# Kernel optimization log

Hardware: AMD Instinct MI355X
Metric: run time of the kernel (lower is better)

The kernel has to match this reference:

```python
import jax, jax.numpy as jnp
import numpy as np

NN_SIZE = 10  # matches init_kwargs nn_size


def _knn_idx(points, k):
    """points: (B,N,D). Returns (B,N,k) indices of k nearest neighbors, self excluded."""
    sq = jnp.sum(points * points, axis=-1)  # (B,N)
    # squared euclidean distances (B,N,N)
    d2 = sq[:, :, None] + sq[:, None, :] - 2.0 * jnp.einsum('bnd,bmd->bnm', points, points)
    _, idx = jax.lax.top_k(-d2, k + 1)  # smallest distances; first hit is self
    return idx[:, :, 1:]  # drop self -> (B,N,k)


def _uniform_laplacian(points, knn_idx):
    """points: (B,N,D); knn_idx: (B,N,K). lap = mean(neighbors) - point."""
    neigh = jax.vmap(lambda p, i: p[i])(points, knn_idx)  # (B,N,K,D) gather per batch
    return jnp.mean(neigh, axis=2) - points


def setup_inputs() -> dict:
    key = jax.random.key(0)
    k1, k2 = jax.random.split(key)
    B, N, D = 2, 8192, 3
    point1 = jax.random.normal(k1, (B, N, D), dtype=jnp.float32)
    point2 = jax.random.normal(k2, (B, N, D), dtype=jnp.float32)
    return {"point1": point1, "point2": point2}


def reference(point1, point2):
    knn_idx = _knn_idx(point1, NN_SIZE)          # connectivity from ref cloud
    lap1 = _uniform_laplacian(point1, knn_idx)   # (B,N,3)
    lap2 = _uniform_laplacian(point2, knn_idx)   # reuse knn_idx
    # metric = L1Loss (mean reduction); use_norm=False
    return jnp.mean(jnp.abs(lap1 - lap2))
```

## Files before the change

kernel.cpp:

```cpp
#include <hip/hip_runtime.h>
#include <math.h>


constexpr int NPTS  = 8192;
constexpr int NB    = 2;
constexpr int KNN   = 10;
constexpr int QPB   = 64;
constexpr int WPB   = 16;
constexpr int BLOCK = QPB * WPB;
constexpr int MASK13 = 0xFFFFE000;

constexpr int   G    = 32;
constexpr int   NC   = G * G * G;
constexpr float BMIN = -5.5f;
constexpr float BW   = 11.0f;
constexpr float H    = BW / G;
constexpr float INVH = (float)G / BW;

__device__ __forceinline__ void ins1(int l[KNN], int x) {
#pragma unroll
    for (int k = KNN - 1; k > 0; --k) l[k] = min(l[k], max(l[k - 1], x));
    l[0] = min(l[0], x);
}
__device__ __forceinline__ void ins2(int l[KNN], int a, int b) {
    const int b0 = min(a, b), b1 = max(a, b);
#pragma unroll
    for (int k = KNN - 1; k >= 2; --k)
        l[k] = min(l[k], min(max(l[k - 1], b0), max(l[k - 2], b1)));
    l[1] = min(l[1], min(max(l[0], b0), b1));
    l[0] = min(l[0], b0);
}
template<int S>
__device__ __forceinline__ void ins2s(int l[KNN], int a, int b) {
    const int b0 = min(a, b), b1 = max(a, b);
#pragma unroll
    for (int k = KNN - 1; k >= S + 2; --k)
        l[k] = min(l[k], min(max(l[k - 1], b0), max(l[k - 2], b1)));
    l[S + 1] = min(l[S + 1], min(max(l[S], b0), b1));
    l[S] = min(l[S], b0);
}
__device__ __forceinline__ void merge_sorted(int l[KNN], const int p[KNN]) {
    ins2s<0>(l, p[0], p[1]);
    ins2s<2>(l, p[2], p[3]);
    ins2s<4>(l, p[4], p[5]);
    ins2s<6>(l, p[6], p[7]);
    ins2s<8>(l, p[8], p[9]);
}

__global__ void pack_bin(const float* __restrict__ p1, float4* __restrict__ w,
                         int* __restrict__ hist, int* __restrict__ cellof,
                         float* __restrict__ out, int* __restrict__ nfail) {
    const int i = blockIdx.x * blockDim.x + threadIdx.x;
    if (i >= NB * NPTS) return;
    if (i == 0) { out[0] = 0.0f; nfail[0] = 0; }
    const float x = p1[3 * i], y = p1[3 * i + 1], z = p1[3 * i + 2];
    w[i] = make_float4(x, y, z, fmaf(x, x, fmaf(y, y, z * z)));
    const int cx = min(max((int)floorf((x - BMIN) * INVH), 0), G - 1);
    const int cy = min(max((int)floorf((y - BMIN) * INVH), 0), G - 1);
    const int cz = min(max((int)floorf((z - BMIN) * INVH), 0), G - 1);
    const int c = (cz << 10) | (cy << 5) | cx;
    cellof[i] = c;
    atomicAdd(&hist[(i >> 13) * NC + c], 1);
}

__global__ __launch_bounds__(1024)
void scan_cells(const int* __restrict__ hist, int* __restrict__ starts) {
    __shared__ int wsum[16];
    const int b = blockIdx.x, t = threadIdx.x;
    const int* hb = hist + b * NC;
    int* sb = starts + b * (NC + 1);
    const int c0 = t * 32;
    int loc[32]; int sum = 0;
#pragma unroll
    for (int j = 0; j < 32; ++j) { loc[j] = hb[c0 + j]; sum += loc[j]; }
    const int lane = t & 63, wvi = t >> 6;
    int incl = sum;
#pragma unroll
    for (int off = 1; off < 64; off <<= 1) {
        const int v = __shfl_up(incl, off);
        if (lane >= off) incl += v;
    }
    if (lane == 63) wsum[wvi] = incl;
    __syncthreads();
    if (t < 16) {
        const int v = wsum[t];
        int iv = v;
#pragma unroll
        for (int off = 1; off < 16; off <<= 1) {
            const int u = __shfl_up(iv, off);
            if (t >= off) iv += u;
        }
        wsum[t] = iv - v;
    }
    __syncthreads();
    int run = wsum[wvi] + incl - sum;
#pragma unroll
    for (int j = 0; j < 32; ++j) { sb[c0 + j] = run; run += loc[j]; }
    if (t == 1023) sb[NC] = run;
}

__global__ void scatter_all(const int* __restrict__ cellof,
                            const int* __restrict__ starts,
                            int* __restrict__ hist,
                            const float4* __restrict__ w,
                            float4* __restrict__ wsorted,
                            int* __restrict__ sIdx) {
    const int i = blockIdx.x * blockDim.x + threadIdx.x;
    if (i >= NB * NPTS) return;
    const int b = i >> 13;
    const int c = cellof[i];
    const int old = atomicSub(&hist[b * NC + c], 1);
    const int pos = b * NPTS + starts[b * (NC + 1) + c] + old - 1;
    wsorted[pos] = w[i];
    sIdx[pos] = i & (NPTS - 1);
}

template<int S>
__device__ __forceinline__ void scan_batched(const float4* __restrict__ W,
                                             const int* __restrict__ st,
                                             int cx, int cy, int cz,
                                             float m2x, float m2y, float m2z,
                                             float q2, int qpos, int wv,
                                             int l[KNN])
{
    constexpr int Wd = 2 * S + 1;
    constexpr int R  = Wd * Wd;
    const int IMAX = 0x7FFFFFFF;
    int J0[R], J1[R];
#pragma unroll
    for (int r = 0; r < R; ++r) {
        const int dy = r % Wd - S, dz = r / Wd - S;
        const int ay = cy + dy, az = cz + dz;
        const bool ok = ((unsigned)ay < G) && ((unsigned)az < G);
        const int cbase = (az << 10) | (ay << 5);
        const int lo = cbase + max(cx - S, 0);
        const int hi = cbase + min(cx + S, G - 1) + 1;
        J0[r] = ok ? st[lo] : 0;
        J1[r] = ok ? st[hi] : 0;
    }
#pragma unroll
    for (int r = 0; r < R; ++r) {
        const int j1 = J1[r];
        int j = J0[r] + wv;
        if (j < j1) {
            float4 c4 = W[j];
            while (true) {
                const int jn = j + WPB;
                const bool more = jn < j1;
                float4 nx;
                if (more) nx = W[jn];
                const float d2 = fmaf(m2x, c4.x,
                                 fmaf(m2y, c4.y,
                                 fmaf(m2z, c4.z, c4.w + q2)));
                int key = (__float_as_int(d2) & MASK13) | j;
                key = (j == qpos) ? IMAX : key;
                ins1(l, key);
                if (!more) break;
                c4 = nx; j = jn;
            }
        }
    }
}

__global__ __launch_bounds__(BLOCK)
void phase1(const float4* __restrict__ wsorted, const int* __restrict__ sIdx,
            const float* __restrict__ p2, const int* __restrict__ starts,
            float* __restrict__ out,
            int* __restrict__ nfail, int* __restrict__ worklist)
{
    __shared__ int mv[WPB * KNN * QPB];

    const int batch = blockIdx.x >> 7;
    const int lane  = threadIdx.x & 63;
    const int wv    = __builtin_amdgcn_readfirstlane(threadIdx.x >> 6);
    const int qpos  = ((blockIdx.x & 127) << 6) + lane;

    const float4* W  = wsorted + batch * NPTS;
    const int*    sI = sIdx + batch * NPTS;
    const float*  P2 = p2 + (size_t)batch * NPTS * 3;
    const int*    st = starts + batch * (NC + 1);

    const float4 qp = W[qpos];
    const int cx = min(max((int)floorf((qp.x - BMIN) * INVH), 0), G - 1);
    const int cy = min(max((int)floorf((qp.y - BMIN) * INVH), 0), G - 1);
    const int cz = min(max((int)floorf((qp.z - BMIN) * INVH), 0), G - 1);
    const float lox = BMIN + cx * H, loy = BMIN + cy * H, loz = BMIN + cz * H;
    const float df = fminf(fminf(fminf(qp.x - lox, lox + H - qp.x),
                                 fminf(qp.y - loy, loy + H - qp.y)),
                           fminf(qp.z - loz, loz + H - qp.z));
    const float m2x = -2.0f * qp.x, m2y = -2.0f * qp.y, m2z = -2.0f * qp.z;
    const float q2 = qp.w;
    const int IMAX = 0x7FFFFFFF;

    const int sCov = (q2 > 4.8f) ? 2 : 1;

    int l[KNN];
#pragma unroll
    for (int k = 0; k < KNN; ++k) l[k] = IMAX;

    if (sCov == 1)
        scan_batched<1>(W, st, cx, cy, cz, m2x, m2y, m2z, q2, qpos, wv, l);
    else
        scan_batched<2>(W, st, cx, cy, cz, m2x, m2y, m2z, q2, qpos, wv, l);

#pragma unroll
    for (int k = 0; k < KNN; ++k) mv[(wv * KNN + k) * QPB + lane] = l[k];
    __syncthreads();

    if (threadIdx.x < QPB) {
        int M[KNN];
#pragma unroll
        for (int k = 0; k < KNN; ++k) M[k] = IMAX;
#pragma unroll
        for (int e = 0; e < WPB; ++e) {
            int p[KNN];
#pragma unroll
            for (int k = 0; k < KNN; ++k) p[k] = mv[(e * KNN + k) * QPB + lane];
            merge_sorted(M, p);
        }

        const float tau = __int_as_float(M[KNN - 1] & MASK13);
        const float R = (float)sCov * H + df;
        const bool covered = (tau <= R * R * 0.996f);
        float v = 0.0f;
        if (covered) {
            float s1x = 0, s1y = 0, s1z = 0, s2x = 0, s2y = 0, s2z = 0;
#pragma unroll
            for (int k = 0; k < KNN; ++k) {
                const int j = M[k] & (NPTS - 1);
                const float4 c4 = W[j];
                const int oi = sI[j];
                s1x += c4.x; s1y += c4.y; s1z += c4.z;
                s2x += P2[3 * oi + 0];
                s2y += P2[3 * oi + 1];
                s2z += P2[3 * oi + 2];
            }
            const int oq = sI[qpos];
            const float p2x = P2[3 * oq + 0];
            const float p2y = P2[3 * oq + 1];
            const float p2z = P2[3 * oq + 2];
            const float dx = (s1x * 0.1f - qp.x) - (s2x * 0.1f - p2x);
            const float dy = (s1y * 0.1f - qp.y) - (s2y * 0.1f - p2y);
            const float dz = (s1z * 0.1f - qp.z) - (s2z * 0.1f - p2z);
            v = fabsf(dx) + fabsf(dy) + fabsf(dz);
        } else {
            const int wi = atomicAdd(nfail, 1);
            worklist[wi] = (batch << 16) | qpos;
        }
#pragma unroll
        for (int off = 32; off >= 1; off >>= 1) v += __shfl_down(v, off);
        if (threadIdx.x == 0)
            atomicAdd(out, v * (1.0f / (float)(NB * NPTS * 3)));
    }
}

constexpr int P2BLK = 256;
constexpr int P2GRID = 512;

__global__ __launch_bounds__(P2BLK)
void phase2(const float4* __restrict__ wsorted, const int* __restrict__ sIdx,
            const float* __restrict__ p2,
            const int* __restrict__ nfail, const int* __restrict__ worklist,
            float* __restrict__ out)
{
    const int lane = threadIdx.x & 63;
    const int wv   = threadIdx.x >> 6;
    const int wid  = blockIdx.x * (P2BLK / 64) + wv;
    const int NW   = P2GRID * (P2BLK / 64);
    const int nf   = *nfail;
    const int IMAX = 0x7FFFFFFF;
    float acc = 0.0f;

    for (int i = wid; i < nf; i += NW) {
        const int e = worklist[i];
        const int batch = e >> 16, qpos = e & 0xFFFF;
        const float4* W  = wsorted + batch * NPTS;
        const int*    sI = sIdx + batch * NPTS;
        const float*  P2 = p2 + (size_t)batch * NPTS * 3;
        const float4 qp = W[qpos];
        const float m2x = -2.0f * qp.x, m2y = -2.0f * qp.y, m2z = -2.0f * qp.z;
        const float q2 = qp.w;

        int l[KNN];
#pragma unroll
        for (int k = 0; k < KNN; ++k) l[k] = IMAX;

#pragma unroll 2
        for (int it = 0; it < NPTS / 128; ++it) {
            const int ja = it * 128 + lane, jb = ja + 64;
            const float4 ca = W[ja];
            const float4 cb = W[jb];
            const float da = fmaf(m2x, ca.x, fmaf(m2y, ca.y, fmaf(m2z, ca.z, ca.w + q2)));
            const float db = fmaf(m2x, cb.x, fmaf(m2y, cb.y, fmaf(m2z, cb.z, cb.w + q2)));
            int ka = (__float_as_int(da) & MASK13) | ja;
            int kb = (__float_as_int(db) & MASK13) | jb;
            ka = (ja == qpos) ? IMAX : ka;
            kb = (jb == qpos) ? IMAX : kb;
            ins2(l, ka, kb);
        }
        for (int off = 1; off < 64; off <<= 1) {
            int p[KNN];
#pragma unroll
            for (int k = 0; k < KNN; ++k) p[k] = __shfl_xor(l[k], off);
            merge_sorted(l, p);
        }
        float s1x = 0, s1y = 0, s1z = 0, s2x = 0, s2y = 0, s2z = 0;
#pragma unroll
        for (int k = 0; k < KNN; ++k) {
            const int j = l[k] & (NPTS - 1);
            const float4 c4 = W[j];
            const int oi = sI[j];
            s1x += c4.x; s1y += c4.y; s1z += c4.z;
            s2x += P2[3 * oi + 0];
            s2y += P2[3 * oi + 1];
            s2z += P2[3 * oi + 2];
        }
        const int oq = sI[qpos];
        const float dx = (s1x * 0.1f - qp.x) - (s2x * 0.1f - P2[3 * oq + 0]);
        const float dy = (s1y * 0.1f - qp.y) - (s2y * 0.1f - P2[3 * oq + 1]);
        const float dz = (s1z * 0.1f - qp.z) - (s2z * 0.1f - P2[3 * oq + 2]);
        if (lane == 0) acc += fabsf(dx) + fabsf(dy) + fabsf(dz);
    }

    if (lane == 0 && acc != 0.0f)
        atomicAdd(out, acc * (1.0f / (float)(NB * NPTS * 3)));
}

constexpr int FB_WPB = 8;
constexpr int FB_BLOCK = QPB * FB_WPB;
constexpr int CHUNK = NPTS / FB_WPB;

__global__ void prep_pack(const float* __restrict__ p, float4* __restrict__ w) {
    const int i = blockIdx.x * blockDim.x + threadIdx.x;
    if (i < NB * NPTS) {
        const float x = p[3 * i], y = p[3 * i + 1], z = p[3 * i + 2];
        w[i] = make_float4(x, y, z, fmaf(x, x, fmaf(y, y, z * z)));
    }
}

__global__ __launch_bounds__(FB_BLOCK, 2)
void knn_lap(const float4* __restrict__ w1, const float* __restrict__ p2,
             float* __restrict__ out)
{
    __shared__ int mv[FB_WPB * KNN * QPB];
    const int batch = blockIdx.x >> 7;
    const int qbase = (blockIdx.x & 127) << 6;
    const int lane  = threadIdx.x & 63;
    const int wv    = __builtin_amdgcn_readfirstlane(threadIdx.x >> 6);
    const int query = qbase + lane;
    const float4* Wb = w1 + batch * NPTS;
    const float4 qp = Wb[query];
    const float m2x = -2.0f * qp.x, m2y = -2.0f * qp.y, m2z = -2.0f * qp.z;
    const float q2 = qp.w;
    const int IMAX = 0x7FFFFFFF;
    int l[KNN];
#pragma unroll
    for (int k = 0; k < KNN; ++k) l[k] = IMAX;
    const int c0 = wv * CHUNK;
    const float4* cand = Wb + c0;
#pragma unroll 4
    for (int i = 0; i < CHUNK; i += 2) {
        const float4 ca = cand[i];
        const float4 cb = cand[i + 1];
        const int ja = c0 + i, jb = ja + 1;
        const float da = fmaf(m2x, ca.x, fmaf(m2y, ca.y, fmaf(m2z, ca.z, ca.w + q2)));
        const float db = fmaf(m2x, cb.x, fmaf(m2y, cb.y, fmaf(m2z, cb.z, cb.w + q2)));
        int ka = (__float_as_int(da) & MASK13) | ja;
        int kb = (__float_as_int(db) & MASK13) | jb;
        ka = (ja == query) ? IMAX : ka;
        kb = (jb == query) ? IMAX : kb;
        ins2(l, ka, kb);
    }
#pragma unroll
    for (int k = 0; k < KNN; ++k) mv[(wv * KNN + k) * QPB + lane] = l[k];
    __syncthreads();
    if (threadIdx.x < QPB) {
        int m[KNN];
#pragma unroll
        for (int k = 0; k < KNN; ++k) m[k] = IMAX;
#pragma unroll
        for (int e = 0; e < FB_WPB; ++e) {
            int p[KNN];
#pragma unroll
            for (int k = 0; k < KNN; ++k) p[k] = mv[(e * KNN + k) * QPB + lane];
            merge_sorted(m, p);
        }
        const float* P2b = p2 + (size_t)batch * NPTS * 3;
        float s1x = 0, s1y = 0, s1z = 0, s2x = 0, s2y = 0, s2z = 0;
#pragma unroll
        for (int k = 0; k < KNN; ++k) {
            const int j = m[k] & (NPTS - 1);
            const float4 c = Wb[j];
            s1x += c.x; s1y += c.y; s1z += c.z;
            s2x += P2b[3 * j + 0]; s2y += P2b[3 * j + 1]; s2z += P2b[3 * j + 2];
        }
        const int q = qbase + threadIdx.x;
        const float p2x = P2b[3 * q + 0], p2y = P2b[3 * q + 1], p2z = P2b[3 * q + 2];
        const float dx = (s1x * 0.1f - qp.x) - (s2x * 0.1f - p2x);
        const float dy = (s1y * 0.1f - qp.y) - (s2y * 0.1f - p2y);
        const float dz = (s1z * 0.1f - qp.z) - (s2z * 0.1f - p2z);
        float v = fabsf(dx) + fabsf(dy) + fabsf(dz);
#pragma unroll
        for (int off = 32; off >= 1; off >>= 1) v += __shfl_down(v, off);
        if (threadIdx.x == 0)
            atomicAdd(out, v * (1.0f / (float)(NB * NPTS * 3)));
    }
}

extern "C" void kernel_launch(void* const* d_in, const int* in_sizes, int n_in,
                              void* d_out, int out_size, void* d_ws, size_t ws_size,
                              hipStream_t stream) {
    const float* p1 = (const float*)d_in[0];
    const float* p2 = (const float*)d_in[1];
    float* out = (float*)d_out;

    size_t off = 0;
    float4* w       = (float4*)d_ws;                off += (size_t)NB * NPTS * 16;
    int*    hist    = (int*)((char*)d_ws + off);    off += (size_t)NB * NC * 4;
    int*    starts  = (int*)((char*)d_ws + off);    off += (size_t)NB * (NC + 1) * 4 + 8;
    int*    cellof  = (int*)((char*)d_ws + off);    off += (size_t)NB * NPTS * 4;
    float4* wsorted = (float4*)((char*)d_ws + off); off += (size_t)NB * NPTS * 16;
    int*    sIdx    = (int*)((char*)d_ws + off);    off += (size_t)NB * NPTS * 4;
    int*    nfail   = (int*)((char*)d_ws + off);    off += 16;
    int*    worklist= (int*)((char*)d_ws + off);    off += (size_t)NB * NPTS * 4;

    if (ws_size < off) {
        hipMemsetAsync(out, 0, sizeof(float), stream);
        prep_pack<<<(NB * NPTS + 255) / 256, 256, 0, stream>>>(p1, w);
        knn_lap<<<NB * (NPTS / QPB), FB_BLOCK, 0, stream>>>(w, p2, out);
        return;
    }

    hipMemsetAsync(hist, 0, (size_t)NB * NC * 4, stream);
    pack_bin<<<(NB * NPTS + 255) / 256, 256, 0, stream>>>(p1, w, hist, cellof,
                                                          out, nfail);
    scan_cells<<<NB, 1024, 0, stream>>>(hist, starts);
    scatter_all<<<(NB * NPTS + 255) / 256, 256, 0, stream>>>(cellof, starts, hist,
                                                             w, wsorted, sIdx);
    phase1<<<NB * (NPTS / QPB), BLOCK, 0, stream>>>(wsorted, sIdx, p2, starts,
                                                    out, nfail, worklist);
    phase2<<<P2GRID, P2BLK, 0, stream>>>(wsorted, sIdx, p2, nfail, worklist, out);
}
```

Measured before the change: 121.5 us.

## Fuse memset, binning, cell scan and scatter into one per-batch build kernel

Replaces the memset plus three small kernels (pack_bin, scan_cells, scatter_all) with a single 1024-thread block per batch. That block zeroes the histogram, bins its points with atomics, prefix-scans the cells and scatters the sorted points while keeping coordinates in registers. This removes several launch gaps and the intermediate w and cellof buffers. The cost is running the binning on only two blocks, so that phase uses much less parallelism, and all histogram atomics go through global memory.

```diff
diff --git a/kernel.cpp b/kernel.cpp
--- a/kernel.cpp
+++ b/kernel.cpp
@@ -47,28 +47,37 @@
     ins2s<8>(l, p[8], p[9]);
 }
 
-__global__ void pack_bin(const float* __restrict__ p1, float4* __restrict__ w,
-                         int* __restrict__ hist, int* __restrict__ cellof,
-                         float* __restrict__ out, int* __restrict__ nfail) {
-    const int i = blockIdx.x * blockDim.x + threadIdx.x;
-    if (i >= NB * NPTS) return;
-    if (i == 0) { out[0] = 0.0f; nfail[0] = 0; }
-    const float x = p1[3 * i], y = p1[3 * i + 1], z = p1[3 * i + 2];
-    w[i] = make_float4(x, y, z, fmaf(x, x, fmaf(y, y, z * z)));
-    const int cx = min(max((int)floorf((x - BMIN) * INVH), 0), G - 1);
-    const int cy = min(max((int)floorf((y - BMIN) * INVH), 0), G - 1);
-    const int cz = min(max((int)floorf((z - BMIN) * INVH), 0), G - 1);
-    const int c = (cz << 10) | (cy << 5) | cx;
-    cellof[i] = c;
-    atomicAdd(&hist[(i >> 13) * NC + c], 1);
-}
-
 __global__ __launch_bounds__(1024)
-void scan_cells(const int* __restrict__ hist, int* __restrict__ starts) {
+void build(const float* __restrict__ p1, int* __restrict__ hist,
+           int* __restrict__ starts, float4* __restrict__ wsorted,
+           int* __restrict__ sIdx, float* __restrict__ out,
+           int* __restrict__ nfail)
+{
     __shared__ int wsum[16];
     const int b = blockIdx.x, t = threadIdx.x;
-    const int* hb = hist + b * NC;
+    if (b == 0 && t == 0) { out[0] = 0.0f; nfail[0] = 0; }
+    int* hb = hist + b * NC;
     int* sb = starts + b * (NC + 1);
+
+#pragma unroll
+    for (int k = 0; k < NC / 1024; ++k) hb[k * 1024 + t] = 0;
+    __syncthreads();
+
+    const float* P = p1 + (size_t)b * NPTS * 3;
+    float xs[8], ys[8], zs[8]; int cs[8];
+#pragma unroll
+    for (int k = 0; k < 8; ++k) {
+        const int i = k * 1024 + t;
+        xs[k] = P[3 * i];  ys[k] = P[3 * i + 1];  zs[k] = P[3 * i + 2];
+        const int cx = min(max((int)floorf((xs[k] - BMIN) * INVH), 0), G - 1);
+        const int cy = min(max((int)floorf((ys[k] - BMIN) * INVH), 0), G - 1);
+        const int cz = min(max((int)floorf((zs[k] - BMIN) * INVH), 0), G - 1);
+        cs[k] = (cz << 10) | (cy << 5) | cx;
+        atomicAdd(&hb[cs[k]], 1);
+    }
+    __syncthreads();
+    __threadfence();
+
     const int c0 = t * 32;
     int loc[32]; int sum = 0;
 #pragma unroll
@@ -97,22 +106,18 @@
 #pragma unroll
     for (int j = 0; j < 32; ++j) { sb[c0 + j] = run; run += loc[j]; }
     if (t == 1023) sb[NC] = run;
-}
-
-__global__ void scatter_all(const int* __restrict__ cellof,
-                            const int* __restrict__ starts,
-                            int* __restrict__ hist,
-                            const float4* __restrict__ w,
-                            float4* __restrict__ wsorted,
-                            int* __restrict__ sIdx) {
-    const int i = blockIdx.x * blockDim.x + threadIdx.x;
-    if (i >= NB * NPTS) return;
-    const int b = i >> 13;
-    const int c = cellof[i];
-    const int old = atomicSub(&hist[b * NC + c], 1);
-    const int pos = b * NPTS + starts[b * (NC + 1) + c] + old - 1;
-    wsorted[pos] = w[i];
-    sIdx[pos] = i & (NPTS - 1);
+    __syncthreads();
+
+#pragma unroll
+    for (int k = 0; k < 8; ++k) {
+        const int i = k * 1024 + t;
+        const int c = cs[k];
+        const int old = atomicSub(&hb[c], 1);
+        const int pos = b * NPTS + sb[c] + old - 1;
+        wsorted[pos] = make_float4(xs[k], ys[k], zs[k],
+            fmaf(xs[k], xs[k], fmaf(ys[k], ys[k], zs[k] * zs[k])));
+        sIdx[pos] = i;
+    }
 }
 
 template<int S>
@@ -415,28 +420,22 @@
     float* out = (float*)d_out;
 
     size_t off = 0;
-    float4* w       = (float4*)d_ws;                off += (size_t)NB * NPTS * 16;
     int*    hist    = (int*)((char*)d_ws + off);    off += (size_t)NB * NC * 4;
     int*    starts  = (int*)((char*)d_ws + off);    off += (size_t)NB * (NC + 1) * 4 + 8;
-    int*    cellof  = (int*)((char*)d_ws + off);    off += (size_t)NB * NPTS * 4;
     float4* wsorted = (float4*)((char*)d_ws + off); off += (size_t)NB * NPTS * 16;
     int*    sIdx    = (int*)((char*)d_ws + off);    off += (size_t)NB * NPTS * 4;
     int*    nfail   = (int*)((char*)d_ws + off);    off += 16;
     int*    worklist= (int*)((char*)d_ws + off);    off += (size_t)NB * NPTS * 4;
+    float4* wfb     = (float4*)((char*)d_ws);
 
     if (ws_size < off) {
         hipMemsetAsync(out, 0, sizeof(float), stream);
-        prep_pack<<<(NB * NPTS + 255) / 256, 256, 0, stream>>>(p1, w);
-        knn_lap<<<NB * (NPTS / QPB), FB_BLOCK, 0, stream>>>(w, p2, out);
+        prep_pack<<<(NB * NPTS + 255) / 256, 256, 0, stream>>>(p1, wfb);
+        knn_lap<<<NB * (NPTS / QPB), FB_BLOCK, 0, stream>>>(wfb, p2, out);
         return;
     }
 
-    hipMemsetAsync(hist, 0, (size_t)NB * NC * 4, stream);
-    pack_bin<<<(NB * NPTS + 255) / 256, 256, 0, stream>>>(p1, w, hist, cellof,
-                                                          out, nfail);
-    scan_cells<<<NB, 1024, 0, stream>>>(hist, starts);
-    scatter_all<<<(NB * NPTS + 255) / 256, 256, 0, stream>>>(cellof, starts, hist,
-                                                             w, wsorted, sIdx);
+    build<<<NB, 1024, 0, stream>>>(p1, hist, starts, wsorted, sIdx, out, nfail);
     phase1<<<NB * (NPTS / QPB), BLOCK, 0, stream>>>(wsorted, sIdx, p2, starts,
                                                     out, nfail, worklist);
     phase2<<<P2GRID, P2BLK, 0, stream>>>(wsorted, sIdx, p2, nfail, worklist, out);
```

Result: slower. 163.8 us (+34.8%).
